# Optimization experiments

Hardware: AMD Instinct MI355X
Metric: run time of the kernel (lower is better)

Reference implementation:

```python
import jax, jax.numpy as jnp
import numpy as np

EMB = 768
HEADS = 8
HEAD_DIM = EMB // HEADS  # 96
SCALING = HEAD_DIM ** -0.5


def setup_inputs() -> dict:
    key = jax.random.key(0)
    ks = jax.random.split(key, 9)
    B, S = 2, 2048
    std = 1.0 / np.sqrt(EMB)
    x = jax.random.normal(ks[0], (B, S, EMB), dtype=jnp.float32)
    # torch nn.Linear weights are [out, in]; we store [in, out] for x @ W.
    Wq = jax.random.normal(ks[1], (EMB, EMB), dtype=jnp.float32) * std
    Wk = jax.random.normal(ks[2], (EMB, EMB), dtype=jnp.float32) * std
    Wv = jax.random.normal(ks[3], (EMB, EMB), dtype=jnp.float32) * std
    Wo = jax.random.normal(ks[4], (EMB, EMB), dtype=jnp.float32) * std
    bq = jax.random.normal(ks[5], (EMB,), dtype=jnp.float32) * std
    bk = jax.random.normal(ks[6], (EMB,), dtype=jnp.float32) * std
    bv = jax.random.normal(ks[7], (EMB,), dtype=jnp.float32) * std
    bo = jax.random.normal(ks[8], (EMB,), dtype=jnp.float32) * std
    return {"x": x, "Wq": Wq, "bq": bq, "Wk": Wk, "bk": bk,
            "Wv": Wv, "bv": bv, "Wo": Wo, "bo": bo}


def _split_heads(t):
    # [B, S, E] -> [B, H, S, D]
    B, S, _ = t.shape
    return t.reshape(B, S, HEADS, HEAD_DIM).transpose(0, 2, 1, 3)


def reference(x, Wq, bq, Wk, bk, Wv, bv, Wo, bo):
    q = _split_heads(x @ Wq + bq)
    k = _split_heads(x @ Wk + bk)
    v = _split_heads(x @ Wv + bv)
    # Full [B, H, S, S] score matrix, as in the source module.
    energies = jnp.einsum('bhqd,bhkd->bhqk', q, k)
    # Faithful quirk: softmax first, THEN multiply by scaling (dropout=0 -> identity).
    attention = jax.nn.softmax(energies, axis=-1) * SCALING
    out = jnp.einsum('bhqk,bhkd->bhqd', attention, v)
    B, H, S, D = out.shape
    out = out.transpose(0, 2, 1, 3).reshape(B, S, H * D)
    return out @ Wo + bo
```

## Files before the change

kernel.cpp:

```cpp
#include <hip/hip_runtime.h>
#include <hip/hip_bf16.h>

#define EMB 768
#define HD 96
#define NH 8
#define SEQ 2048
#define SCALING 0.10206207261596575f

typedef short bf16x8 __attribute__((ext_vector_type(8)));
typedef float f32x4  __attribute__((ext_vector_type(4)));
typedef unsigned short u16v8 __attribute__((ext_vector_type(8)));
typedef unsigned short u16v4 __attribute__((ext_vector_type(4)));

union F4 { float4 v; float f[4]; };

__device__ __forceinline__ unsigned short f2bf(float v) {
    __hip_bfloat16 b = __float2bfloat16(v);
    return *reinterpret_cast<unsigned short*>(&b);
}
__device__ __forceinline__ float bf2f(unsigned short u) {
    __hip_bfloat16 b = *reinterpret_cast<__hip_bfloat16*>(&u);
    return __bfloat162float(b);
}

__device__ __forceinline__ void dma16(const unsigned short* g, unsigned short* l) {
    __builtin_amdgcn_global_load_lds(
        (const __attribute__((address_space(1))) unsigned int*)g,
        (__attribute__((address_space(3))) unsigned int*)l,
        16, 0, 0);
}

__global__ __launch_bounds__(256) void convert_x(
    const float* __restrict__ x,
    unsigned short* __restrict__ xh, unsigned short* __restrict__ xl)
{
    const size_t i0 = ((size_t)blockIdx.x * 256 + threadIdx.x) * 8;
    F4 a, b;
    a.v = *(const float4*)&x[i0];
    b.v = *(const float4*)&x[i0 + 4];
    u16v8 h, l;
    #pragma unroll
    for (int j = 0; j < 4; j++) {
        unsigned short hu = f2bf(a.f[j]);
        h[j] = hu; l[j] = f2bf(a.f[j] - bf2f(hu));
    }
    #pragma unroll
    for (int j = 0; j < 4; j++) {
        unsigned short hu = f2bf(b.f[j]);
        h[4+j] = hu; l[4+j] = f2bf(b.f[j] - bf2f(hu));
    }
    *(u16v8*)&xh[i0] = h;
    *(u16v8*)&xl[i0] = l;
}

__global__ __launch_bounds__(256) void convert_wT(
    const float* __restrict__ Wq, const float* __restrict__ Wk,
    const float* __restrict__ Wv, const float* __restrict__ Wo,
    unsigned short* __restrict__ WhT, unsigned short* __restrict__ WlT)
{
    const int z = blockIdx.z;
    const float* W = (z == 0) ? Wq : (z == 1) ? Wk : (z == 2) ? Wv : Wo;
    unsigned short* oh = WhT + (size_t)z * 589824;
    unsigned short* ol = WlT + (size_t)z * 589824;
    __shared__ float T[64][68];
    const int t = threadIdx.x;
    const int r = t >> 2, cg = (t & 3) * 16;
    const int k0 = blockIdx.x * 64, n0 = blockIdx.y * 64;
    #pragma unroll
    for (int i = 0; i < 4; i++) {
        float4 v = *(const float4*)&W[(size_t)(k0 + r) * EMB + n0 + cg + 4*i];
        *(float4*)&T[r][cg + 4*i] = v;
    }
    __syncthreads();
    #pragma unroll
    for (int i = 0; i < 4; i++) {
        u16v4 h, l;
        #pragma unroll
        for (int j = 0; j < 4; j++) {
            float v = T[cg + 4*i + j][r];
            unsigned short hu = f2bf(v);
            h[j] = hu; l[j] = f2bf(v - bf2f(hu));
        }
        *(u16v4*)&oh[(size_t)(n0 + r) * EMB + k0 + cg + 4*i] = h;
        *(u16v4*)&ol[(size_t)(n0 + r) * EMB + k0 + cg + 4*i] = l;
    }
}

#define QA_H 0
#define QA_L 4096
#define QW_H 8192
#define QW_L 12288

__global__ __launch_bounds__(256, 3) void qkv_mfma(
    const unsigned short* __restrict__ xh, const unsigned short* __restrict__ xl,
    const unsigned short* __restrict__ WhT, const unsigned short* __restrict__ WlT,
    const float* __restrict__ bq, const float* __restrict__ bk, const float* __restrict__ bv,
    unsigned short* __restrict__ Qh, unsigned short* __restrict__ Ql,
    unsigned short* __restrict__ Kb, unsigned short* __restrict__ Vt)
{
    const int which = blockIdx.z;
    const unsigned short* Wh = WhT + (size_t)which * 589824;
    const unsigned short* Wl = WlT + (size_t)which * 589824;
    const float* bias = (which == 0) ? bq : (which == 1) ? bk : bv;

    __shared__ __align__(16) unsigned short lds[16384];
    const int tid = threadIdx.x;
    const int lane = tid & 63, lo = lane & 15, h4 = lane >> 4;
    const int w = tid >> 6, wm = w & 1, wn = w >> 1;
    const int row0 = blockIdx.x * 128, col0 = blockIdx.y * 128;

    const unsigned short* sbase =
        (w == 0) ? xh + (size_t)row0 * EMB :
        (w == 1) ? xl + (size_t)row0 * EMB :
        (w == 2) ? Wh + (size_t)col0 * EMB :
                   Wl + (size_t)col0 * EMB;
    const int soff = w * 4096;

    f32x4 acc[4][4];
    #pragma unroll
    for (int i = 0; i < 4; i++)
        #pragma unroll
        for (int j = 0; j < 4; j++) acc[i][j] = (f32x4){0.f, 0.f, 0.f, 0.f};

    for (int k0 = 0; k0 < EMB; k0 += 32) {
        #pragma unroll
        for (int j = 0; j < 8; j++) {
            const int u = j*64 + lane;
            const int row = u >> 2, c8 = (u & 3) * 8;
            dma16(sbase + (size_t)row * EMB + k0 + c8, &lds[soff + j*512]);
        }
        __syncthreads();

        bf16x8 ah[4], al[4];
        #pragma unroll
        for (int i = 0; i < 4; i++)
            ah[i] = *(const bf16x8*)&lds[QA_H + (64*wm + 16*i + lo)*32 + 8*h4];
        if (which <= 1) {
            #pragma unroll
            for (int i = 0; i < 4; i++)
                al[i] = *(const bf16x8*)&lds[QA_L + (64*wm + 16*i + lo)*32 + 8*h4];
        }
        #pragma unroll
        for (int j = 0; j < 4; j++) {
            bf16x8 whf = *(const bf16x8*)&lds[QW_H + (64*wn + 16*j + lo)*32 + 8*h4];
            #pragma unroll
            for (int i = 0; i < 4; i++)
                acc[i][j] = __builtin_amdgcn_mfma_f32_16x16x32_bf16(ah[i], whf, acc[i][j], 0, 0, 0);
            if (which <= 1) {
                #pragma unroll
                for (int i = 0; i < 4; i++)
                    acc[i][j] = __builtin_amdgcn_mfma_f32_16x16x32_bf16(al[i], whf, acc[i][j], 0, 0, 0);
            }
            if (which != 1) {
                bf16x8 wlf = *(const bf16x8*)&lds[QW_L + (64*wn + 16*j + lo)*32 + 8*h4];
                #pragma unroll
                for (int i = 0; i < 4; i++)
                    acc[i][j] = __builtin_amdgcn_mfma_f32_16x16x32_bf16(ah[i], wlf, acc[i][j], 0, 0, 0);
            }
        }
        __syncthreads();
    }

    if (which == 0) {
        #pragma unroll
        for (int i = 0; i < 4; i++)
            #pragma unroll
            for (int r = 0; r < 4; r++) {
                const int sg = row0 + 64*wm + 16*i + 4*h4 + r;
                const int b = sg >> 11, s = sg & 2047;
                #pragma unroll
                for (int j = 0; j < 4; j++) {
                    const int c = col0 + 64*wn + 16*j + lo;
                    const int h = c / HD, d = c - h*HD;
                    float v = acc[i][j][r] + bias[c];
                    unsigned short hu = f2bf(v);
                    const size_t base = ((size_t)(b*NH + h) * SEQ + s) * HD + d;
                    Qh[base] = hu;
                    Ql[base] = f2bf(v - bf2f(hu));
                }
            }
    } else if (which == 1) {
        #pragma unroll
        for (int i = 0; i < 4; i++)
            #pragma unroll
            for (int r = 0; r < 4; r++) {
                const int sg = row0 + 64*wm + 16*i + 4*h4 + r;
                const int b = sg >> 11, s = sg & 2047;
                #pragma unroll
                for (int j = 0; j < 4; j++) {
                    const int c = col0 + 64*wn + 16*j + lo;
                    const int h = c / HD, d = c - h*HD;
                    float v = acc[i][j][r] + bias[c];
                    Kb[((size_t)(b*NH + h) * SEQ + s) * HD + d] = f2bf(v);
                }
            }
    } else {
        #pragma unroll
        for (int i = 0; i < 4; i++)
            #pragma unroll
            for (int r = 0; r < 4; r++) {
                const int sg = row0 + 64*wm + 16*i + 4*h4 + r;
                const int b = sg >> 11, s = sg & 2047;
                #pragma unroll
                for (int j = 0; j < 4; j++) {
                    const int c = col0 + 64*wn + 16*j + lo;
                    const int h = c / HD, d = c - h*HD;
                    float v = acc[i][j][r] + bias[c];
                    Vt[((size_t)(b*NH + h) * HD + d) * SEQ + s] = f2bf(v);
                }
            }
    }
}

#define PA_O 0
#define PWH_O 4096
#define PWL_O 6144

__global__ __launch_bounds__(256, 3) void proj_mfma(
    const unsigned short* __restrict__ AOh,
    const unsigned short* __restrict__ Wh, const unsigned short* __restrict__ Wl,
    const float* __restrict__ bo, float* __restrict__ out)
{
    __shared__ __align__(16) unsigned short lds[8192];
    const int tid = threadIdx.x;
    const int lane = tid & 63, lo = lane & 15, h4 = lane >> 4;
    const int w = tid >> 6, wm = w & 1, wn = w >> 1;
    const int row0 = blockIdx.x * 128, col0 = blockIdx.y * 64;

    const unsigned short* sbase =
        (w <= 1) ? AOh + (size_t)row0 * EMB :
        (w == 2) ? Wh  + (size_t)col0 * EMB :
                   Wl  + (size_t)col0 * EMB;
    const int jbase = (w == 1) ? 4 : 0;
    const int soff  = (w <= 1) ? PA_O : (w == 2) ? PWH_O : PWL_O;

    f32x4 acc[4][2];
    #pragma unroll
    for (int i = 0; i < 4; i++)
        #pragma unroll
        for (int j = 0; j < 2; j++) acc[i][j] = (f32x4){0.f, 0.f, 0.f, 0.f};

    for (int k0 = 0; k0 < EMB; k0 += 32) {
        #pragma unroll
        for (int jj = 0; jj < 4; jj++) {
            const int j = jbase + jj;
            const int u = j*64 + lane;
            const int row = u >> 2, c8 = (u & 3) * 8;
            dma16(sbase + (size_t)row * EMB + k0 + c8, &lds[soff + j*512]);
        }
        __syncthreads();

        bf16x8 af[4];
        #pragma unroll
        for (int i = 0; i < 4; i++)
            af[i] = *(const bf16x8*)&lds[PA_O + (64*wm + 16*i + lo)*32 + 8*h4];
        #pragma unroll
        for (int j = 0; j < 2; j++) {
            bf16x8 whf = *(const bf16x8*)&lds[PWH_O + (32*wn + 16*j + lo)*32 + 8*h4];
            bf16x8 wlf = *(const bf16x8*)&lds[PWL_O + (32*wn + 16*j + lo)*32 + 8*h4];
            #pragma unroll
            for (int i = 0; i < 4; i++) {
                acc[i][j] = __builtin_amdgcn_mfma_f32_16x16x32_bf16(af[i], whf, acc[i][j], 0, 0, 0);
                acc[i][j] = __builtin_amdgcn_mfma_f32_16x16x32_bf16(af[i], wlf, acc[i][j], 0, 0, 0);
            }
        }
        __syncthreads();
    }

    #pragma unroll
    for (int i = 0; i < 4; i++)
        #pragma unroll
        for (int r = 0; r < 4; r++) {
            const int sg = row0 + 64*wm + 16*i + 4*h4 + r;
            #pragma unroll
            for (int j = 0; j < 2; j++) {
                const int c = col0 + 32*wn + 16*j + lo;
                out[(size_t)sg * EMB + c] = acc[i][j][r] + bo[c];
            }
        }
}

#define ACH 13568
#define APAIR 27136
#define AP_OFF 54272

__global__ __launch_bounds__(512, 2) void attn_mfma(
    const unsigned short* __restrict__ Qh, const unsigned short* __restrict__ Ql,
    const unsigned short* __restrict__ Kb, const unsigned short* __restrict__ Vt,
    unsigned short* __restrict__ AOh)
{
    __shared__ __align__(16) unsigned short lds[72704];
    const int id   = blockIdx.x;
    const int xcd  = id & 7;
    const int j    = id >> 3;
    const int bh   = 2*xcd + (j & 1);
    const int q0   = (j >> 1) * 128;
    const int tid  = threadIdx.x;
    const int w    = tid >> 6;
    const int g    = w >> 2;
    const int wq   = w & 3;
    const int lane = tid & 63;
    const int lo   = lane & 15;
    const int h4   = lane >> 4;

    const unsigned short* KbH = Kb + (size_t)bh * SEQ * HD;
    const unsigned short* VtH = Vt + (size_t)bh * HD * SEQ;

    const unsigned short* sp0[6];
    int fK[6];
    int doff[6];
    #pragma unroll
    for (int r = 0; r < 6; r++) {
        const int e  = tid + 512*r;
        const int ch = (e >= 1536) ? 1 : 0;
        const int e2 = e - ch*1536;
        if (e2 < 768) {
            const int kk = e2 / 12, g8 = e2 - kk*12;
            sp0[r]  = KbH + (size_t)(ch*64 + kk) * HD + 8*g8;
            fK[r]   = HD;
            doff[r] = ch*ACH + kk*104 + 8*g8;
        } else {
            const int uv = e2 - 768, dV = uv >> 3, c8 = uv & 7;
            sp0[r]  = VtH + (size_t)dV*SEQ + ch*64 + 8*c8;
            fK[r]   = 1;
            doff[r] = ch*ACH + 6656 + dV*72 + 8*c8;
        }
    }

    bf16x8 qhf[2][3], qlf[2][3];
    #pragma unroll
    for (int mi = 0; mi < 2; mi++) {
        const size_t qoff = ((size_t)bh*SEQ + q0 + 32*wq + 16*mi + lo) * HD + 8*h4;
        #pragma unroll
        for (int ks = 0; ks < 3; ks++) {
            qhf[mi][ks] = *(const bf16x8*)&Qh[qoff + 32*ks];
            qlf[mi][ks] = *(const bf16x8*)&Ql[qoff + 32*ks];
        }
    }

    f32x4 O[2][6];
    #pragma unroll
    for (int mi = 0; mi < 2; mi++)
        #pragma unroll
        for (int i = 0; i < 6; i++) O[mi][i] = (f32x4){0.f, 0.f, 0.f, 0.f};
    float lsum[2][4] = {};

    unsigned short* Pw = lds + AP_OFF + w * 2304;

    #pragma unroll
    for (int r = 0; r < 6; r++)
        *(u16v8*)&lds[doff[r]] = *(const u16v8*)sp0[r];
    __syncthreads();

    #pragma unroll 1
    for (int u = 0; u < 16; u++) {
        const int kn0 = (u < 15) ? 128*(u + 1) : 0;
        u16v8 st[6];
        #pragma unroll
        for (int r = 0; r < 6; r++)
            st[r] = *(const u16v8*)(sp0[r] + (size_t)kn0 * fK[r]);

        const unsigned short* myK = lds + (u & 1)*APAIR + g*ACH;
        const unsigned short* myV = myK + 6656;

        f32x4 S[2][4];
        #pragma unroll
        for (int mi = 0; mi < 2; mi++)
            #pragma unroll
            for (int nb = 0; nb < 4; nb++) S[mi][nb] = (f32x4){0.f, 0.f, 0.f, 0.f};
        #pragma unroll
        for (int ks = 0; ks < 3; ks++) {
            bf16x8 kf[4];
            #pragma unroll
            for (int nb = 0; nb < 4; nb++)
                kf[nb] = *(const bf16x8*)&myK[(16*nb + lo)*104 + 32*ks + 8*h4];
            #pragma unroll
            for (int nb = 0; nb < 4; nb++)
                #pragma unroll
                for (int mi = 0; mi < 2; mi++) {
                    S[mi][nb] = __builtin_amdgcn_mfma_f32_16x16x32_bf16(qhf[mi][ks], kf[nb], S[mi][nb], 0, 0, 0);
                    S[mi][nb] = __builtin_amdgcn_mfma_f32_16x16x32_bf16(qlf[mi][ks], kf[nb], S[mi][nb], 0, 0, 0);
                }
        }

        #pragma unroll
        for (int mi = 0; mi < 2; mi++)
            #pragma unroll
            for (int nb = 0; nb < 4; nb++)
                #pragma unroll
                for (int r = 0; r < 4; r++) {
                    float p = __expf(S[mi][nb][r]);
                    lsum[mi][r] += p;
                    Pw[(16*mi + 4*h4 + r)*72 + 16*nb + lo] = f2bf(p);
                }

        #pragma unroll
        for (int ks2 = 0; ks2 < 2; ks2++) {
            bf16x8 pf0 = *(const bf16x8*)&Pw[(lo)*72      + 32*ks2 + 8*h4];
            bf16x8 pf1 = *(const bf16x8*)&Pw[(16 + lo)*72 + 32*ks2 + 8*h4];
            #pragma unroll
            for (int nb2 = 0; nb2 < 6; nb2++) {
                bf16x8 vfv = *(const bf16x8*)&myV[(16*nb2 + lo)*72 + 32*ks2 + 8*h4];
                O[0][nb2] = __builtin_amdgcn_mfma_f32_16x16x32_bf16(pf0, vfv, O[0][nb2], 0, 0, 0);
                O[1][nb2] = __builtin_amdgcn_mfma_f32_16x16x32_bf16(pf1, vfv, O[1][nb2], 0, 0, 0);
            }
        }

        unsigned short* dstp = lds + ((u + 1) & 1)*APAIR;
        #pragma unroll
        for (int r = 0; r < 6; r++)
            *(u16v8*)&dstp[doff[r]] = st[r];
        __syncthreads();
    }

    float* Fo = (float*)lds;
    float* Ls = (float*)lds + 12288;
    if (g == 1) {
        #pragma unroll
        for (int mi = 0; mi < 2; mi++)
            #pragma unroll
            for (int r = 0; r < 4; r++) {
                const int ql = 32*wq + 16*mi + 4*h4 + r;
                Ls[ql*16 + lo] = lsum[mi][r];
                #pragma unroll
                for (int nb2 = 0; nb2 < 6; nb2++)
                    Fo[ql*96 + 16*nb2 + lo] = O[mi][nb2][r];
            }
    }
    __syncthreads();
    if (g == 0) {
        const int b = bh >> 3, hh = bh & 7;
        #pragma unroll
        for (int mi = 0; mi < 2; mi++)
            #pragma unroll
            for (int r = 0; r < 4; r++) {
                const int ql = 32*wq + 16*mi + 4*h4 + r;
                float l = lsum[mi][r] + Ls[ql*16 + lo];
                l += __shfl_xor(l, 1);
                l += __shfl_xor(l, 2);
                l += __shfl_xor(l, 4);
                l += __shfl_xor(l, 8);
                const float sc = SCALING / l;
                const int q = q0 + ql;
                const size_t base = ((size_t)b*SEQ + q)*EMB + hh*HD + lo;
                #pragma unroll
                for (int nb2 = 0; nb2 < 6; nb2++)
                    AOh[base + 16*nb2] = f2bf((O[mi][nb2][r] + Fo[ql*96 + 16*nb2 + lo]) * sc);
            }
    }
}

extern "C" void kernel_launch(void* const* d_in, const int* in_sizes, int n_in,
                              void* d_out, int out_size, void* d_ws, size_t ws_size,
                              hipStream_t stream)
{
    const float* x  = (const float*)d_in[0];
    const float* Wq = (const float*)d_in[1];
    const float* bq = (const float*)d_in[2];
    const float* Wk = (const float*)d_in[3];
    const float* bk = (const float*)d_in[4];
    const float* Wv = (const float*)d_in[5];
    const float* bv = (const float*)d_in[6];
    const float* Wo = (const float*)d_in[7];
    const float* bo = (const float*)d_in[8];
    float* out = (float*)d_out;

    unsigned short* ws = (unsigned short*)d_ws;
    const size_t HS = (size_t)16 * SEQ * HD;
    const size_t WS1 = (size_t)EMB * EMB;
    unsigned short* Qh  = ws;
    unsigned short* Ql  = ws + HS;
    unsigned short* Kb  = ws + 2*HS;
    unsigned short* Vt  = ws + 3*HS;
    unsigned short* xh  = ws + 4*HS;
    unsigned short* xl  = ws + 5*HS;
    unsigned short* WhT = ws + 6*HS;
    unsigned short* WlT = ws + 6*HS + 4*WS1;
    unsigned short* AOh = xh;

    convert_x<<<1536, 256, 0, stream>>>(x, xh, xl);
    convert_wT<<<dim3(12, 12, 4), 256, 0, stream>>>(Wq, Wk, Wv, Wo, WhT, WlT);
    qkv_mfma<<<dim3(32, 6, 3), 256, 0, stream>>>(xh, xl, WhT, WlT, bq, bk, bv,
                                                 Qh, Ql, Kb, Vt);
    attn_mfma<<<256, 512, 0, stream>>>(Qh, Ql, Kb, Vt, AOh);
    proj_mfma<<<dim3(32, 12), 256, 0, stream>>>(AOh, WhT + 3*WS1, WlT + 3*WS1, bo, out);
}
```

Before: 206.0 us.

## Halve GEMM row tiles for more blocks and add MFMA priority hints in attention

Result: slower. 262.0 us (+27.2%).

```diff
diff --git a/kernel.cpp b/kernel.cpp
--- a/kernel.cpp
+++ b/kernel.cpp
@@ -87,11 +87,11 @@
 }
 
 #define QA_H 0
-#define QA_L 4096
-#define QW_H 8192
-#define QW_L 12288
-
-__global__ __launch_bounds__(256, 3) void qkv_mfma(
+#define QA_L 2048
+#define QW_H 4096
+#define QW_L 8192
+
+__global__ __launch_bounds__(256, 6) void qkv_mfma(
     const unsigned short* __restrict__ xh, const unsigned short* __restrict__ xl,
     const unsigned short* __restrict__ WhT, const unsigned short* __restrict__ WlT,
     const float* __restrict__ bq, const float* __restrict__ bk, const float* __restrict__ bv,
@@ -103,58 +103,56 @@
     const unsigned short* Wl = WlT + (size_t)which * 589824;
     const float* bias = (which == 0) ? bq : (which == 1) ? bk : bv;
 
-    __shared__ __align__(16) unsigned short lds[16384];
+    __shared__ __align__(16) unsigned short lds[12288];
     const int tid = threadIdx.x;
     const int lane = tid & 63, lo = lane & 15, h4 = lane >> 4;
     const int w = tid >> 6, wm = w & 1, wn = w >> 1;
-    const int row0 = blockIdx.x * 128, col0 = blockIdx.y * 128;
-
-    const unsigned short* sbase =
-        (w == 0) ? xh + (size_t)row0 * EMB :
-        (w == 1) ? xl + (size_t)row0 * EMB :
-        (w == 2) ? Wh + (size_t)col0 * EMB :
-                   Wl + (size_t)col0 * EMB;
-    const int soff = w * 4096;
-
-    f32x4 acc[4][4];
-    #pragma unroll
-    for (int i = 0; i < 4; i++)
+    const int row0 = blockIdx.x * 64, col0 = blockIdx.y * 128;
+    const int r16 = lane >> 2, c8 = (lane & 3) * 8;
+
+    f32x4 acc[2][4];
+    #pragma unroll
+    for (int i = 0; i < 2; i++)
         #pragma unroll
         for (int j = 0; j < 4; j++) acc[i][j] = (f32x4){0.f, 0.f, 0.f, 0.f};
 
     for (int k0 = 0; k0 < EMB; k0 += 32) {
         #pragma unroll
-        for (int j = 0; j < 8; j++) {
-            const int u = j*64 + lane;
-            const int row = u >> 2, c8 = (u & 3) * 8;
-            dma16(sbase + (size_t)row * EMB + k0 + c8, &lds[soff + j*512]);
+        for (int jj = 0; jj < 6; jj++) {
+            const int u = w*6 + jj;
+            const unsigned short* g; int ld;
+            if (u < 4)       { g = xh + (size_t)(row0 + u*16      + r16) * EMB + k0 + c8; ld = QA_H + u*512; }
+            else if (u < 8)  { g = xl + (size_t)(row0 + (u-4)*16  + r16) * EMB + k0 + c8; ld = QA_L + (u-4)*512; }
+            else if (u < 16) { g = Wh + (size_t)(col0 + (u-8)*16  + r16) * EMB + k0 + c8; ld = QW_H + (u-8)*512; }
+            else             { g = Wl + (size_t)(col0 + (u-16)*16 + r16) * EMB + k0 + c8; ld = QW_L + (u-16)*512; }
+            dma16(g, &lds[ld]);
         }
         __syncthreads();
 
-        bf16x8 ah[4], al[4];
-        #pragma unroll
-        for (int i = 0; i < 4; i++)
-            ah[i] = *(const bf16x8*)&lds[QA_H + (64*wm + 16*i + lo)*32 + 8*h4];
+        bf16x8 ah[2], al[2];
+        #pragma unroll
+        for (int i = 0; i < 2; i++)
+            ah[i] = *(const bf16x8*)&lds[QA_H + (32*wm + 16*i + lo)*32 + 8*h4];
         if (which <= 1) {
             #pragma unroll
-            for (int i = 0; i < 4; i++)
-                al[i] = *(const bf16x8*)&lds[QA_L + (64*wm + 16*i + lo)*32 + 8*h4];
+            for (int i = 0; i < 2; i++)
+                al[i] = *(const bf16x8*)&lds[QA_L + (32*wm + 16*i + lo)*32 + 8*h4];
         }
         #pragma unroll
         for (int j = 0; j < 4; j++) {
             bf16x8 whf = *(const bf16x8*)&lds[QW_H + (64*wn + 16*j + lo)*32 + 8*h4];
             #pragma unroll
-            for (int i = 0; i < 4; i++)
+            for (int i = 0; i < 2; i++)
                 acc[i][j] = __builtin_amdgcn_mfma_f32_16x16x32_bf16(ah[i], whf, acc[i][j], 0, 0, 0);
             if (which <= 1) {
                 #pragma unroll
-                for (int i = 0; i < 4; i++)
+                for (int i = 0; i < 2; i++)
                     acc[i][j] = __builtin_amdgcn_mfma_f32_16x16x32_bf16(al[i], whf, acc[i][j], 0, 0, 0);
             }
             if (which != 1) {
                 bf16x8 wlf = *(const bf16x8*)&lds[QW_L + (64*wn + 16*j + lo)*32 + 8*h4];
                 #pragma unroll
-                for (int i = 0; i < 4; i++)
+                for (int i = 0; i < 2; i++)
                     acc[i][j] = __builtin_amdgcn_mfma_f32_16x16x32_bf16(ah[i], wlf, acc[i][j], 0, 0, 0);
             }
         }
@@ -163,10 +161,10 @@
 
     if (which == 0) {
         #pragma unroll
-        for (int i = 0; i < 4; i++)
+        for (int i = 0; i < 2; i++)
             #pragma unroll
             for (int r = 0; r < 4; r++) {
-                const int sg = row0 + 64*wm + 16*i + 4*h4 + r;
+                const int sg = row0 + 32*wm + 16*i + 4*h4 + r;
                 const int b = sg >> 11, s = sg & 2047;
                 #pragma unroll
                 for (int j = 0; j < 4; j++) {
@@ -181,10 +179,10 @@
             }
     } else if (which == 1) {
         #pragma unroll
-        for (int i = 0; i < 4; i++)
+        for (int i = 0; i < 2; i++)
             #pragma unroll
             for (int r = 0; r < 4; r++) {
-                const int sg = row0 + 64*wm + 16*i + 4*h4 + r;
+                const int sg = row0 + 32*wm + 16*i + 4*h4 + r;
                 const int b = sg >> 11, s = sg & 2047;
                 #pragma unroll
                 for (int j = 0; j < 4; j++) {
@@ -196,10 +194,10 @@
             }
     } else {
         #pragma unroll
-        for (int i = 0; i < 4; i++)
+        for (int i = 0; i < 2; i++)
             #pragma unroll
             for (int r = 0; r < 4; r++) {
-                const int sg = row0 + 64*wm + 16*i + 4*h4 + r;
+                const int sg = row0 + 32*wm + 16*i + 4*h4 + r;
                 const int b = sg >> 11, s = sg & 2047;
                 #pragma unroll
                 for (int j = 0; j < 4; j++) {
@@ -213,53 +211,49 @@
 }
 
 #define PA_O 0
-#define PWH_O 4096
-#define PWL_O 6144
+#define PWH_O 2048
+#define PWL_O 4096
 
 __global__ __launch_bounds__(256, 3) void proj_mfma(
     const unsigned short* __restrict__ AOh,
     const unsigned short* __restrict__ Wh, const unsigned short* __restrict__ Wl,
     const float* __restrict__ bo, float* __restrict__ out)
 {
-    __shared__ __align__(16) unsigned short lds[8192];
+    __shared__ __align__(16) unsigned short lds[6144];
     const int tid = threadIdx.x;
     const int lane = tid & 63, lo = lane & 15, h4 = lane >> 4;
     const int w = tid >> 6, wm = w & 1, wn = w >> 1;
-    const int row0 = blockIdx.x * 128, col0 = blockIdx.y * 64;
-
-    const unsigned short* sbase =
-        (w <= 1) ? AOh + (size_t)row0 * EMB :
-        (w == 2) ? Wh  + (size_t)col0 * EMB :
-                   Wl  + (size_t)col0 * EMB;
-    const int jbase = (w == 1) ? 4 : 0;
-    const int soff  = (w <= 1) ? PA_O : (w == 2) ? PWH_O : PWL_O;
-
-    f32x4 acc[4][2];
-    #pragma unroll
-    for (int i = 0; i < 4; i++)
+    const int row0 = blockIdx.x * 64, col0 = blockIdx.y * 64;
+    const int r16 = lane >> 2, c8 = (lane & 3) * 8;
+
+    f32x4 acc[2][2];
+    #pragma unroll
+    for (int i = 0; i < 2; i++)
         #pragma unroll
         for (int j = 0; j < 2; j++) acc[i][j] = (f32x4){0.f, 0.f, 0.f, 0.f};
 
     for (int k0 = 0; k0 < EMB; k0 += 32) {
         #pragma unroll
-        for (int jj = 0; jj < 4; jj++) {
-            const int j = jbase + jj;
-            const int u = j*64 + lane;
-            const int row = u >> 2, c8 = (u & 3) * 8;
-            dma16(sbase + (size_t)row * EMB + k0 + c8, &lds[soff + j*512]);
+        for (int jj = 0; jj < 3; jj++) {
+            const int u = w*3 + jj;
+            const unsigned short* g; int ld;
+            if (u < 4)      { g = AOh + (size_t)(row0 + u*16     + r16) * EMB + k0 + c8; ld = PA_O  + u*512; }
+            else if (u < 8) { g = Wh  + (size_t)(col0 + (u-4)*16 + r16) * EMB + k0 + c8; ld = PWH_O + (u-4)*512; }
+            else            { g = Wl  + (size_t)(col0 + (u-8)*16 + r16) * EMB + k0 + c8; ld = PWL_O + (u-8)*512; }
+            dma16(g, &lds[ld]);
         }
         __syncthreads();
 
-        bf16x8 af[4];
-        #pragma unroll
-        for (int i = 0; i < 4; i++)
-            af[i] = *(const bf16x8*)&lds[PA_O + (64*wm + 16*i + lo)*32 + 8*h4];
+        bf16x8 af[2];
+        #pragma unroll
+        for (int i = 0; i < 2; i++)
+            af[i] = *(const bf16x8*)&lds[PA_O + (32*wm + 16*i + lo)*32 + 8*h4];
         #pragma unroll
         for (int j = 0; j < 2; j++) {
             bf16x8 whf = *(const bf16x8*)&lds[PWH_O + (32*wn + 16*j + lo)*32 + 8*h4];
             bf16x8 wlf = *(const bf16x8*)&lds[PWL_O + (32*wn + 16*j + lo)*32 + 8*h4];
             #pragma unroll
-            for (int i = 0; i < 4; i++) {
+            for (int i = 0; i < 2; i++) {
                 acc[i][j] = __builtin_amdgcn_mfma_f32_16x16x32_bf16(af[i], whf, acc[i][j], 0, 0, 0);
                 acc[i][j] = __builtin_amdgcn_mfma_f32_16x16x32_bf16(af[i], wlf, acc[i][j], 0, 0, 0);
             }
@@ -268,10 +262,10 @@
     }
 
     #pragma unroll
-    for (int i = 0; i < 4; i++)
+    for (int i = 0; i < 2; i++)
         #pragma unroll
         for (int r = 0; r < 4; r++) {
-            const int sg = row0 + 64*wm + 16*i + 4*h4 + r;
+            const int sg = row0 + 32*wm + 16*i + 4*h4 + r;
             #pragma unroll
             for (int j = 0; j < 2; j++) {
                 const int c = col0 + 32*wn + 16*j + lo;
@@ -368,6 +362,7 @@
         for (int mi = 0; mi < 2; mi++)
             #pragma unroll
             for (int nb = 0; nb < 4; nb++) S[mi][nb] = (f32x4){0.f, 0.f, 0.f, 0.f};
+        __builtin_amdgcn_s_setprio(1);
         #pragma unroll
         for (int ks = 0; ks < 3; ks++) {
             bf16x8 kf[4];
@@ -382,6 +377,7 @@
                     S[mi][nb] = __builtin_amdgcn_mfma_f32_16x16x32_bf16(qlf[mi][ks], kf[nb], S[mi][nb], 0, 0, 0);
                 }
         }
+        __builtin_amdgcn_s_setprio(0);
 
         #pragma unroll
         for (int mi = 0; mi < 2; mi++)
@@ -394,6 +390,7 @@
                     Pw[(16*mi + 4*h4 + r)*72 + 16*nb + lo] = f2bf(p);
                 }
 
+        __builtin_amdgcn_s_setprio(1);
         #pragma unroll
         for (int ks2 = 0; ks2 < 2; ks2++) {
             bf16x8 pf0 = *(const bf16x8*)&Pw[(lo)*72      + 32*ks2 + 8*h4];
@@ -405,6 +402,7 @@
                 O[1][nb2] = __builtin_amdgcn_mfma_f32_16x16x32_bf16(pf1, vfv, O[1][nb2], 0, 0, 0);
             }
         }
+        __builtin_amdgcn_s_setprio(0);
 
         unsigned short* dstp = lds + ((u + 1) & 1)*APAIR;
         #pragma unroll
@@ -480,8 +478,8 @@
 
     convert_x<<<1536, 256, 0, stream>>>(x, xh, xl);
     convert_wT<<<dim3(12, 12, 4), 256, 0, stream>>>(Wq, Wk, Wv, Wo, WhT, WlT);
-    qkv_mfma<<<dim3(32, 6, 3), 256, 0, stream>>>(xh, xl, WhT, WlT, bq, bk, bv,
+    qkv_mfma<<<dim3(64, 6, 3), 256, 0, stream>>>(xh, xl, WhT, WlT, bq, bk, bv,
                                                  Qh, Ql, Kb, Vt);
     attn_mfma<<<256, 512, 0, stream>>>(Qh, Ql, Kb, Vt, AOh);
-    proj_mfma<<<dim3(32, 12), 256, 0, stream>>>(AOh, WhT + 3*WS1, WlT + 3*WS1, bo, out);
-}
+    proj_mfma<<<dim3(64, 12), 256, 0, stream>>>(AOh, WhT + 3*WS1, WlT + 3*WS1, bo, out);
+}
```
